# Kernel optimization log

Hardware: AMD Instinct MI355X
Metric: run time of the kernel (lower is better)

Reference implementation:

```python
import jax, jax.numpy as jnp
import numpy as np

F = 2048          # frame length = len(window_function) = n_fft
HOP = F // 2      # step_length (overlap=2, perfect reconstruction)
B = 8             # signals / channels
T = 1 << 20       # samples per signal (multiple of HOP)


def setup_inputs() -> dict:
    key = jax.random.key(0)
    x = jax.random.normal(key, (B, T), dtype=jnp.float32)
    # cosine (sine) window, the standard MDCT deringing window
    n = jnp.arange(F, dtype=jnp.float32)
    window = jnp.sin(jnp.pi * (n + 0.5) / F).astype(jnp.float32)
    return {"x": x, "window": window}


def reference(x, window):
    # Batched, fused version of the serial per-frame twiddle-FFT-twiddle MDCT.
    F_ = window.shape[0]
    hop = F_ // 2
    N = F_ // 2                      # output bins per frame (odd-stacked)
    # center=True: pad F/2 zeros on both sides so first/last frames are centered
    xp = jnp.pad(x, ((0, 0), (hop, hop)))
    n_frames = (xp.shape[1] - F_) // hop + 1
    starts = jnp.arange(n_frames) * hop                       # [nf]
    frames = xp[:, starts[:, None] + jnp.arange(F_)]          # [B, nf, F]
    # pre-twiddle: exp(-i*pi*n/(2N)), n = 0..2N-1
    pre = jnp.exp(-1j * jnp.pi * jnp.arange(F_) / F_).astype(jnp.complex64)
    # post-twiddle: exp(-i*pi*n0*(k+0.5)/N), n0 = (N+1)/2
    n0 = (N + 1) / 2.0
    post = jnp.exp(-1j * jnp.pi * n0 * (jnp.arange(N) + 0.5) / N).astype(jnp.complex64)
    # window + pre-twiddle, one batched FFT over all frames, truncate to N bins
    Xc = jnp.fft.fft((frames * window).astype(jnp.complex64) * pre, axis=-1)[..., :N]
    # real part * post-twiddle phase, scale sqrt(1/N)*sqrt(2)
    out = jnp.real(Xc * post) * np.float32(np.sqrt(2.0 / N))
    return out.astype(jnp.float32)          # [B, n_frames, N]
```

## Files before the change

kernel.cpp:

```cpp
#include <hip/hip_runtime.h>
#include <cmath>

#define BATCH   8
#define TLEN    1048576
#define NFRM    1025
#define MROWS   (BATCH * NFRM)

__global__ __launch_bounds__(256)
void mdct_fft_kernel(const float* __restrict__ x,
                     const float* __restrict__ w,
                     float* __restrict__ out)
{
    __shared__ float  uf[1024];
    __shared__ float2 za[512];
    __shared__ float2 zb[512];

    const int r   = blockIdx.x;
    const int tid = threadIdx.x;
    const int b = r / NFRM;
    const int t = r - b * NFRM;

    {
        const int p = tid * 4;
        const float* xb = x + b * TLEN + (t - 1) * 1024;
        const bool low = (p < 512);
        const bool valid = low ? (t != NFRM - 1) : (t != 0);
        float4 res = {0.0f, 0.0f, 0.0f, 0.0f};
        if (valid) {
            const int rb = 1532 - p;
            const int fb = low ? (1536 + p) : (p - 512);
            float4 xr = *(const float4*)(xb + rb);
            float4 wr = *(const float4*)(w  + rb);
            float4 xf = *(const float4*)(xb + fb);
            float4 wf = *(const float4*)(w  + fb);
            if (low) {
                res.x = -(wr.w * xr.w + wf.x * xf.x);
                res.y = -(wr.z * xr.z + wf.y * xf.y);
                res.z = -(wr.y * xr.y + wf.z * xf.z);
                res.w = -(wr.x * xr.x + wf.w * xf.w);
            } else {
                res.x = wf.x * xf.x - wr.w * xr.w;
                res.y = wf.y * xf.y - wr.z * xr.z;
                res.z = wf.z * xf.z - wr.y * xr.y;
                res.w = wf.w * xf.w - wr.x * xr.x;
            }
        }
        *(float4*)&uf[p] = res;
    }
    __syncthreads();

#pragma unroll
    for (int h = 0; h < 2; ++h) {
        int n = tid + h * 256;
        float re = uf[2 * n];
        float im = uf[1023 - 2 * n];
        float a = (float)(4 * n + 1) * (1.0f / 4096.0f);
        float c = cospif(a), s = sinpif(a);
        za[n] = make_float2(re * c + im * s, im * c - re * s);
    }

    float2* X = za;
    float2* Y = zb;
    int mh = 256;
    int ls = 0;
#pragma unroll
    for (int st = 0; st < 9; ++st) {
        __syncthreads();
        const int s = 1 << ls;
        const int p = tid >> ls;
        float ang = (float)p * (1.0f / (float)mh);
        float c = cospif(ang), sn = sinpif(ang);
        float2 a  = X[tid];
        float2 bv = X[tid + 256];
        float2 sum = make_float2(a.x + bv.x, a.y + bv.y);
        float dx = a.x - bv.x, dy = a.y - bv.y;
        float2 wd = make_float2(dx * c + dy * sn, dy * c - dx * sn);
        Y[tid + s * p]     = sum;
        Y[tid + s * p + s] = wd;
        float2* tmp = X; X = Y; Y = tmp;
        mh >>= 1; ++ls;
    }
    __syncthreads();

#pragma unroll
    for (int h = 0; h < 2; ++h) {
        int k = tid + h * 256;
        float2 Zk = X[k];
        float a = (float)(4 * k + 1) * (1.0f / 4096.0f);
        float c = cospif(a), s = sinpif(a);
        float re = Zk.x * c + Zk.y * s;
        float im = Zk.y * c - Zk.x * s;
        uf[2 * k]        =  re * 0.04419417382415922f;
        uf[1023 - 2 * k] = -im * 0.04419417382415922f;
    }
    __syncthreads();

    *(float4*)&out[r * 1024 + tid * 4] = *(const float4*)&uf[tid * 4];
}

extern "C" void kernel_launch(void* const* d_in, const int* in_sizes, int n_in,
                              void* d_out, int out_size, void* d_ws, size_t ws_size,
                              hipStream_t stream) {
    const float* x = (const float*)d_in[0];
    const float* w = (const float*)d_in[1];
    float* out = (float*)d_out;
    (void)d_ws; (void)ws_size;

    mdct_fft_kernel<<<MROWS, 256, 0, stream>>>(x, w, out);
}
```

Measured before the change: 97.40 us.

## Switch FFT to radix-4 stages with swizzled shared memory and fused final stage

Replaces the nine radix-2 Stockham stages with four radix-4 stages run by 128 threads, plus a final radix-2 stage fused into the post-twiddle. Each radix-4 stage derives its higher twiddles from one sincos by complex multiplication. Shared-memory indices are XOR-swizzled to reduce bank conflicts. This cuts the number of barriers and LDS round trips, but leaves half the threads idle during the radix-4 stages and adds some rounding error from the derived twiddles.

```diff
diff --git a/kernel.cpp b/kernel.cpp
--- a/kernel.cpp
+++ b/kernel.cpp
@@ -5,6 +5,8 @@
 #define TLEN    1048576
 #define NFRM    1025
 #define MROWS   (BATCH * NFRM)
+
+#define SWZ(i) ((i) ^ (((i) >> 4) & 15))
 
 __global__ __launch_bounds__(256)
 void mdct_fft_kernel(const float* __restrict__ x,
@@ -56,42 +58,59 @@
         float im = uf[1023 - 2 * n];
         float a = (float)(4 * n + 1) * (1.0f / 4096.0f);
         float c = cospif(a), s = sinpif(a);
-        za[n] = make_float2(re * c + im * s, im * c - re * s);
+        za[SWZ(n)] = make_float2(re * c + im * s, im * c - re * s);
     }
+    __syncthreads();
 
     float2* X = za;
     float2* Y = zb;
-    int mh = 256;
-    int ls = 0;
 #pragma unroll
-    for (int st = 0; st < 9; ++st) {
+    for (int j = 0; j < 4; ++j) {
+        const int ls = 2 * j;
+        const int s  = 1 << ls;
+        const int mh = 256 >> ls;
+        if (tid < 128) {
+            const int p = tid >> ls;
+            float2 P0 = X[SWZ(tid)];
+            float2 P1 = X[SWZ(tid + 128)];
+            float2 P2 = X[SWZ(tid + 256)];
+            float2 P3 = X[SWZ(tid + 384)];
+            float ang = (float)p * (1.0f / (float)mh);
+            float c1 = cospif(ang), s1 = sinpif(ang);
+            float c2 = c1 * c1 - s1 * s1, s2 = 2.0f * c1 * s1;
+            float c3 = c1 * c2 - s1 * s2, s3 = s1 * c2 + c1 * s2;
+            float sax = P0.x + P2.x, say = P0.y + P2.y;
+            float sbx = P1.x + P3.x, sby = P1.y + P3.y;
+            float dax = P0.x - P2.x, day = P0.y - P2.y;
+            float dbx = P1.x - P3.x, dby = P1.y - P3.y;
+            const int o = tid + 3 * s * p;
+            Y[SWZ(o)] = make_float2(sax + sbx, say + sby);
+            float e1x = dax + dby, e1y = day - dbx;
+            Y[SWZ(o + s)] = make_float2(e1x * c1 + e1y * s1, e1y * c1 - e1x * s1);
+            float e2x = sax - sbx, e2y = say - sby;
+            Y[SWZ(o + 2 * s)] = make_float2(e2x * c2 + e2y * s2, e2y * c2 - e2x * s2);
+            float e3x = dax - dby, e3y = day + dbx;
+            Y[SWZ(o + 3 * s)] = make_float2(e3x * c3 + e3y * s3, e3y * c3 - e3x * s3);
+        }
+        float2* tmp = X; X = Y; Y = tmp;
         __syncthreads();
-        const int s = 1 << ls;
-        const int p = tid >> ls;
-        float ang = (float)p * (1.0f / (float)mh);
-        float c = cospif(ang), sn = sinpif(ang);
-        float2 a  = X[tid];
-        float2 bv = X[tid + 256];
-        float2 sum = make_float2(a.x + bv.x, a.y + bv.y);
-        float dx = a.x - bv.x, dy = a.y - bv.y;
-        float2 wd = make_float2(dx * c + dy * sn, dy * c - dx * sn);
-        Y[tid + s * p]     = sum;
-        Y[tid + s * p + s] = wd;
-        float2* tmp = X; X = Y; Y = tmp;
-        mh >>= 1; ++ls;
     }
-    __syncthreads();
 
+    {
+        float2 A  = X[SWZ(tid)];
+        float2 Bv = X[SWZ(tid + 256)];
+        float zr[2] = {A.x + Bv.x, A.x - Bv.x};
+        float zi[2] = {A.y + Bv.y, A.y - Bv.y};
 #pragma unroll
-    for (int h = 0; h < 2; ++h) {
-        int k = tid + h * 256;
-        float2 Zk = X[k];
-        float a = (float)(4 * k + 1) * (1.0f / 4096.0f);
-        float c = cospif(a), s = sinpif(a);
-        float re = Zk.x * c + Zk.y * s;
-        float im = Zk.y * c - Zk.x * s;
-        uf[2 * k]        =  re * 0.04419417382415922f;
-        uf[1023 - 2 * k] = -im * 0.04419417382415922f;
+        for (int h = 0; h < 2; ++h) {
+            int k = tid + h * 256;
+            float a = (float)(4 * k + 1) * (1.0f / 4096.0f);
+            float c = cospif(a), s = sinpif(a);
+            float re = zr[h] * c + zi[h] * s;
+            float im = zi[h] * c - zr[h] * s;
+            uf[2 * k]        =  re * 0.04419417382415922f;
+            uf[1023 - 2 * k] = -im * 0.04419417382415922f;
+        }
     }
     __syncthreads();
 
```

New measurement: 92.98 us. -4.5%, faster.
